# Kernel tuning notes

Measured on AMD Instinct MI355X. Metric: run time of the kernel, lower is better.

Reference implementation:

```python
import jax, jax.numpy as jnp
import numpy as np

N_NODES = 100000
N_EDGES = 800000
IN_F, H_F, OUT_F = 512, 256, 64
N_EXPERTS = 4  # k = 1


def _normalize_edges(edge_index, n):
    """gcn_norm: add self loops, symmetric D^-1/2 A D^-1/2 edge weights."""
    loop = jnp.arange(n, dtype=edge_index.dtype)
    row = jnp.concatenate([edge_index[0], loop])
    col = jnp.concatenate([edge_index[1], loop])
    w = jnp.ones(row.shape[0], dtype=jnp.float32)
    deg = jax.ops.segment_sum(w, col, num_segments=n)  # in-degree incl. self loop
    dinv = jnp.where(deg > 0, deg ** -0.5, 0.0)
    norm = dinv[row] * w * dinv[col]
    return row, col, norm


def _propagate(x, row, col, norm, n):
    # message x_j * edge_weight, scatter-add at destination col
    msgs = x[row] * norm[:, None]
    return jax.ops.segment_sum(msgs, col, num_segments=n)


def _moe_linear(x, w_gate, expert_w, expert_b):
    # eval-mode noisy top-k gating with k=1: clean logits, top-1, softmax over
    # a single logit -> gate value 1.0 for the selected expert.
    logits = x @ w_gate                         # [N, E]
    idx = jnp.argmax(logits, axis=-1)           # [N]
    gates = jax.nn.one_hot(idx, N_EXPERTS, dtype=x.dtype)  # [N, E]
    y_all = jnp.einsum('ni,eio->neo', x, expert_w) + expert_b[None]  # [N, E, H]
    return jnp.einsum('ne,neo->no', gates, y_all)


def setup_inputs() -> dict:
    key = jax.random.key(0)
    ks = jax.random.split(key, 8)
    x = jax.random.normal(ks[0], (N_NODES, IN_F), dtype=jnp.float32)
    edge_index = jax.random.randint(ks[1], (2, N_EDGES), 0, N_NODES, dtype=jnp.int64)
    w_gate = jax.random.normal(ks[2], (IN_F, N_EXPERTS), dtype=jnp.float32) * 0.05
    expert_w = jax.random.normal(ks[3], (N_EXPERTS, IN_F, H_F), dtype=jnp.float32) * (1.0 / np.sqrt(IN_F))
    expert_b = jnp.zeros((N_EXPERTS, H_F), dtype=jnp.float32)
    bias1 = jnp.zeros((H_F,), dtype=jnp.float32)
    w2 = jax.random.normal(ks[4], (H_F, OUT_F), dtype=jnp.float32) * (1.0 / np.sqrt(H_F))
    bias2 = jnp.zeros((OUT_F,), dtype=jnp.float32)
    return {"x": x, "edge_index": edge_index, "w_gate": w_gate,
            "expert_w": expert_w, "expert_b": expert_b, "bias1": bias1,
            "w2": w2, "bias2": bias2}


def reference(x, edge_index, w_gate, expert_w, expert_b, bias1, w2, bias2):
    n = x.shape[0]
    row, col, norm = _normalize_edges(edge_index, n)
    # conv1: MoE linear -> propagate -> bias
    h = _moe_linear(x, w_gate, expert_w, expert_b)
    h = _propagate(h, row, col, norm, n) + bias1
    h = jax.nn.relu(h)
    # dropout is identity at eval
    # conv2: plain GCNConv
    h = h @ w2
    h = _propagate(h, row, col, norm, n) + bias2
    return jax.nn.log_softmax(h, axis=1)
```

## Files before the change

kernel.cpp:

```cpp
#include <hip/hip_runtime.h>
#include <math.h>

typedef __bf16 bf16x8 __attribute__((ext_vector_type(8)));
typedef float f32x16 __attribute__((ext_vector_type(16)));

__device__ __forceinline__ float wave_reduce_sum(float v) {
  #pragma unroll
  for (int off = 32; off > 0; off >>= 1) v += __shfl_xor(v, off, 64);
  return v;
}
__device__ __forceinline__ float wave_reduce_max(float v) {
  #pragma unroll
  for (int off = 32; off > 0; off >>= 1) v = fmaxf(v, __shfl_xor(v, off, 64));
  return v;
}
__device__ __forceinline__ unsigned short f2bf(float f) {
  union { float f; unsigned int u; } v; v.f = f;
  unsigned int r = (v.u + 0x7FFFu + ((v.u >> 16) & 1u)) >> 16;
  return (unsigned short)r;
}
__device__ __forceinline__ float bf2f(unsigned short u) {
  union { unsigned int u; float f; } v; v.u = ((unsigned int)u) << 16;
  return v.f;
}

__global__ void k_init(int* cnt, int* meta, int N) {
  int i = blockIdx.x * blockDim.x + threadIdx.x;
  if (i < N) cnt[i] = 0;
  if (i < 32) meta[i] = 0;
}

__global__ void k_count(const int* __restrict__ col, int* __restrict__ cnt, int E) {
  int e = blockIdx.x * blockDim.x + threadIdx.x;
  if (e < E) atomicAdd(&cnt[col[e]], 1);
}

__global__ __launch_bounds__(256) void k_scanA(const int* __restrict__ cnt,
                                               int* __restrict__ incl,
                                               int* __restrict__ bsums, int N) {
  __shared__ int s[1024];
  int base = blockIdx.x * 1024;
  #pragma unroll
  for (int t = 0; t < 4; ++t) {
    int i = threadIdx.x + t * 256;
    int idx = base + i;
    s[i] = (idx < N) ? cnt[idx] : 0;
  }
  __syncthreads();
  for (int d = 1; d < 1024; d <<= 1) {
    int v[4];
    #pragma unroll
    for (int t = 0; t < 4; ++t) {
      int i = threadIdx.x + t * 256;
      v[t] = (i >= d) ? s[i - d] : 0;
    }
    __syncthreads();
    #pragma unroll
    for (int t = 0; t < 4; ++t) {
      int i = threadIdx.x + t * 256;
      s[i] += v[t];
    }
    __syncthreads();
  }
  #pragma unroll
  for (int t = 0; t < 4; ++t) {
    int i = threadIdx.x + t * 256;
    int idx = base + i;
    if (idx < N) incl[idx] = s[i];
  }
  if (threadIdx.x == 0) bsums[blockIdx.x] = s[1023];
}

__global__ __launch_bounds__(256) void k_scanB(const int* __restrict__ bsums,
                                               int* __restrict__ boff, int nb) {
  __shared__ int s[1024];
  #pragma unroll
  for (int t = 0; t < 4; ++t) {
    int i = threadIdx.x + t * 256;
    s[i] = (i < nb) ? bsums[i] : 0;
  }
  __syncthreads();
  for (int d = 1; d < 1024; d <<= 1) {
    int v[4];
    #pragma unroll
    for (int t = 0; t < 4; ++t) {
      int i = threadIdx.x + t * 256;
      v[t] = (i >= d) ? s[i - d] : 0;
    }
    __syncthreads();
    #pragma unroll
    for (int t = 0; t < 4; ++t) {
      int i = threadIdx.x + t * 256;
      s[i] += v[t];
    }
    __syncthreads();
  }
  #pragma unroll
  for (int t = 0; t < 4; ++t) {
    int i = threadIdx.x + t * 256;
    if (i < nb) boff[i] = (i == 0) ? 0 : s[i - 1];
  }
}

__global__ void k_scanC(const int* __restrict__ cnt, const int* __restrict__ incl,
                        const int* __restrict__ boff, int* __restrict__ rowptr,
                        int* __restrict__ cursor, float* __restrict__ dinv, int N, int E) {
  int i = blockIdx.x * blockDim.x + threadIdx.x;
  if (i < N) {
    int ex = incl[i] - cnt[i] + boff[i >> 10];
    rowptr[i] = ex;
    cursor[i] = ex;
    dinv[i] = rsqrtf((float)(cnt[i] + 1));
    if (i == 0) rowptr[N] = E;
  }
}

__global__ void k_scatter(const int* __restrict__ row, const int* __restrict__ col,
                          int* __restrict__ cursor, int* __restrict__ csr, int E) {
  int e = blockIdx.x * blockDim.x + threadIdx.x;
  if (e < E) {
    int c = col[e];
    int p = atomicAdd(&cursor[c], 1);
    csr[p] = row[e];
  }
}

__global__ __launch_bounds__(256) void k_gate(const float* __restrict__ x,
                                              const float* __restrict__ wg,
                                              int* __restrict__ eidx,
                                              int* __restrict__ meta,
                                              unsigned short* __restrict__ xb, int N) {
  __shared__ int lhist[4];
  int tid = threadIdx.x;
  if (tid < 4) lhist[tid] = 0;
  __syncthreads();
  int node = blockIdx.x * 16 + (tid >> 4);
  int sl = tid & 15;
  if (node < N) {
    const float* xr = x + (size_t)node * 512;
    unsigned short* xbr = xb + (size_t)node * 512;
    float l0 = 0.f, l1 = 0.f, l2 = 0.f, l3 = 0.f;
    #pragma unroll
    for (int j = 0; j < 8; ++j) {
      int q = sl + 16 * j;
      float4 xv = *(const float4*)(xr + 4 * q);
      ushort4 ov;
      ov.x = f2bf(xv.x); ov.y = f2bf(xv.y); ov.z = f2bf(xv.z); ov.w = f2bf(xv.w);
      *(ushort4*)(xbr + 4 * q) = ov;
      float4 w0 = *(const float4*)(wg + 4 * (4 * q + 0));
      float4 w1 = *(const float4*)(wg + 4 * (4 * q + 1));
      float4 w2 = *(const float4*)(wg + 4 * (4 * q + 2));
      float4 w3 = *(const float4*)(wg + 4 * (4 * q + 3));
      l0 += xv.x * w0.x + xv.y * w1.x + xv.z * w2.x + xv.w * w3.x;
      l1 += xv.x * w0.y + xv.y * w1.y + xv.z * w2.y + xv.w * w3.y;
      l2 += xv.x * w0.z + xv.y * w1.z + xv.z * w2.z + xv.w * w3.z;
      l3 += xv.x * w0.w + xv.y * w1.w + xv.z * w2.w + xv.w * w3.w;
    }
    #pragma unroll
    for (int off = 8; off > 0; off >>= 1) {
      l0 += __shfl_xor(l0, off, 64);
      l1 += __shfl_xor(l1, off, 64);
      l2 += __shfl_xor(l2, off, 64);
      l3 += __shfl_xor(l3, off, 64);
    }
    if (sl == 0) {
      int a = 0; float best = l0;
      if (l1 > best) { best = l1; a = 1; }
      if (l2 > best) { best = l2; a = 2; }
      if (l3 > best) { best = l3; a = 3; }
      eidx[node] = a;
      atomicAdd(&lhist[a], 1);
    }
  }
  __syncthreads();
  if (tid < 4 && lhist[tid] > 0) atomicAdd(&meta[tid], lhist[tid]);
}

__global__ void k_offs(int* meta) {
  if (threadIdx.x == 0 && blockIdx.x == 0) {
    int* hist = meta;
    int* eoff = meta + 4;
    int* toff = meta + 9;
    int* ecur = meta + 14;
    int s = 0, t = 0;
    eoff[0] = 0; toff[0] = 0;
    for (int e = 0; e < 4; ++e) {
      s += hist[e];
      eoff[e + 1] = s;
      t += (hist[e] + 127) / 128;
      toff[e + 1] = t;
      ecur[e] = eoff[e];
    }
  }
}

__global__ __launch_bounds__(256) void k_binscatter(const int* __restrict__ eidx,
                                                    int* __restrict__ meta,
                                                    int* __restrict__ perm, int N) {
  __shared__ int lhist[4];
  __shared__ int lbase[4];
  int tid = threadIdx.x;
  if (tid < 4) lhist[tid] = 0;
  __syncthreads();
  int n = blockIdx.x * 256 + tid;
  int e = 0, lrank = 0;
  bool valid = (n < N);
  if (valid) {
    e = eidx[n];
    lrank = atomicAdd(&lhist[e], 1);
  }
  __syncthreads();
  if (tid < 4) {
    int c = lhist[tid];
    lbase[tid] = (c > 0) ? atomicAdd(&meta[14 + tid], c) : 0;
  }
  __syncthreads();
  if (valid) perm[lbase[e] + lrank] = n;
}

__global__ __launch_bounds__(256) void k_pack(const float* __restrict__ ew,
                                              unsigned short* __restrict__ ewb) {
  int b = blockIdx.x;
  int n = threadIdx.x;
  int e = b >> 6, kc = b & 63;
  const float* src = ew + ((size_t)e * 512 + (size_t)kc * 8) * 256 + n;
  unsigned short tmp[8];
  #pragma unroll
  for (int ke = 0; ke < 8; ++ke) tmp[ke] = f2bf(src[(size_t)ke * 256]);
  *(uint4*)(ewb + ((size_t)b * 256 + n) * 8) = *(const uint4*)tmp;
}

__global__ __launch_bounds__(64) void k_pack2(const float* __restrict__ w2,
                                              unsigned short* __restrict__ w2b) {
  int kc = blockIdx.x;
  int n = threadIdx.x;
  const float* src = w2 + (size_t)kc * 8 * 64 + n;
  unsigned short tmp[8];
  #pragma unroll
  for (int ke = 0; ke < 8; ++ke) tmp[ke] = f2bf(src[(size_t)ke * 64]);
  *(uint4*)(w2b + ((size_t)kc * 64 + n) * 8) = *(const uint4*)tmp;
}

__global__ __launch_bounds__(512, 2) void k_gemm1(const unsigned short* __restrict__ xb,
                                                  const unsigned short* __restrict__ ewb,
                                                  const float* __restrict__ eb,
                                                  const int* __restrict__ perm,
                                                  const int* __restrict__ meta,
                                                  unsigned short* __restrict__ h1) {
  __shared__ __align__(16) unsigned short A_lds[8192];
  __shared__ __align__(16) unsigned short B_lds[16384];
  __shared__ int sperm[128];
  const int* eoff = meta + 4;
  const int* toff = meta + 9;
  int v = blockIdx.x;
  if (v >= toff[4]) return;
  int e = 0;
  while (v >= toff[e + 1]) ++e;
  int m0 = eoff[e] + (v - toff[e]) * 128;
  int mEnd = eoff[e + 1];
  int tid = threadIdx.x;

  if (tid < 128) {
    int m = m0 + tid;
    sperm[tid] = perm[(m < mEnd) ? m : (mEnd - 1)];
  }
  __syncthreads();

  int wave = tid >> 6, lane = tid & 63;
  int wr = wave >> 2, wc = wave & 3;
  int hi = lane >> 5, lo = lane & 31;

  f32x16 acc[2][2];
  #pragma unroll
  for (int mi = 0; mi < 2; ++mi)
    #pragma unroll
    for (int ni = 0; ni < 2; ++ni)
      #pragma unroll
      for (int r = 0; r < 16; ++r) acc[mi][ni][r] = 0.f;

  const unsigned short* arow = xb + (size_t)sperm[tid & 127] * 512;
  int kclA = tid >> 7;
  const uint4* ebase = (const uint4*)(ewb + (size_t)e * 64 * 2048);

  for (int k0 = 0; k0 < 512; k0 += 64) {
    uint4 a0 = *(const uint4*)(arow + k0 + kclA * 8);
    uint4 a1 = *(const uint4*)(arow + k0 + (kclA + 4) * 8);
    const uint4* bsrc = ebase + (size_t)(k0 >> 3) * 256;
    uint4 b0 = bsrc[tid];
    uint4 b1 = bsrc[512 + tid];
    uint4 b2 = bsrc[1024 + tid];
    uint4 b3 = bsrc[1536 + tid];
    __syncthreads();
    *(uint4*)&A_lds[((size_t)kclA * 128 + (tid & 127)) * 8] = a0;
    *(uint4*)&A_lds[((size_t)(kclA + 4) * 128 + (tid & 127)) * 8] = a1;
    *(uint4*)&B_lds[((size_t)0 * 512 + tid) * 8] = b0;
    *(uint4*)&B_lds[((size_t)1 * 512 + tid) * 8] = b1;
    *(uint4*)&B_lds[((size_t)2 * 512 + tid) * 8] = b2;
    *(uint4*)&B_lds[((size_t)3 * 512 + tid) * 8] = b3;
    __syncthreads();
    #pragma unroll
    for (int s = 0; s < 4; ++s) {
      int kcl = s * 2 + hi;
      bf16x8 a0f = *(const bf16x8*)&A_lds[((size_t)kcl * 128 + wr * 64 + lo) * 8];
      bf16x8 a1f = *(const bf16x8*)&A_lds[((size_t)kcl * 128 + wr * 64 + 32 + lo) * 8];
      bf16x8 b0f = *(const bf16x8*)&B_lds[((size_t)kcl * 256 + wc * 64 + lo) * 8];
      bf16x8 b1f = *(const bf16x8*)&B_lds[((size_t)kcl * 256 + wc * 64 + 32 + lo) * 8];
      acc[0][0] = __builtin_amdgcn_mfma_f32_32x32x16_bf16(a0f, b0f, acc[0][0], 0, 0, 0);
      acc[0][1] = __builtin_amdgcn_mfma_f32_32x32x16_bf16(a0f, b1f, acc[0][1], 0, 0, 0);
      acc[1][0] = __builtin_amdgcn_mfma_f32_32x32x16_bf16(a1f, b0f, acc[1][0], 0, 0, 0);
      acc[1][1] = __builtin_amdgcn_mfma_f32_32x32x16_bf16(a1f, b1f, acc[1][1], 0, 0, 0);
    }
  }

  #pragma unroll
  for (int ni = 0; ni < 2; ++ni) {
    int col = wc * 64 + ni * 32 + lo;
    float bias = eb[e * 256 + col];
    #pragma unroll
    for (int mi = 0; mi < 2; ++mi) {
      #pragma unroll
      for (int q = 0; q < 4; ++q) {
        #pragma unroll
        for (int j = 0; j < 4; ++j) {
          int r = j + 8 * q + 4 * hi;
          int lrow = wr * 64 + mi * 32 + r;
          if (m0 + lrow < mEnd) {
            h1[(size_t)sperm[lrow] * 256 + col] = f2bf(acc[mi][ni][q * 4 + j] + bias);
          }
        }
      }
    }
  }
}

__global__ __launch_bounds__(256) void k_prop1(const unsigned short* __restrict__ h1,
                                               const int* __restrict__ rowptr,
                                               const int* __restrict__ csr,
                                               const float* __restrict__ dinv,
                                               const float* __restrict__ bias1,
                                               unsigned short* __restrict__ hrelu, int N) {
  int c = blockIdx.x * 4 + (threadIdx.x >> 6);
  int lane = threadIdx.x & 63;
  if (c >= N) return;
  float dc = dinv[c];
  const ushort4* hr = (const ushort4*)h1;
  ushort4 sv = hr[(size_t)c * 64 + lane];
  float sl = dc * dc;
  float ax = bf2f(sv.x) * sl, ay = bf2f(sv.y) * sl, az = bf2f(sv.z) * sl, aw = bf2f(sv.w) * sl;
  int jb = rowptr[c], je = rowptr[c + 1];
  int j = jb;
  for (; j + 3 < je; j += 4) {
    int r0 = csr[j], r1 = csr[j + 1], r2 = csr[j + 2], r3 = csr[j + 3];
    float s0 = dinv[r0] * dc, s1 = dinv[r1] * dc, s2 = dinv[r2] * dc, s3 = dinv[r3] * dc;
    ushort4 h0 = hr[(size_t)r0 * 64 + lane];
    ushort4 h1v = hr[(size_t)r1 * 64 + lane];
    ushort4 h2 = hr[(size_t)r2 * 64 + lane];
    ushort4 h3v = hr[(size_t)r3 * 64 + lane];
    ax += bf2f(h0.x) * s0; ay += bf2f(h0.y) * s0; az += bf2f(h0.z) * s0; aw += bf2f(h0.w) * s0;
    ax += bf2f(h1v.x) * s1; ay += bf2f(h1v.y) * s1; az += bf2f(h1v.z) * s1; aw += bf2f(h1v.w) * s1;
    ax += bf2f(h2.x) * s2; ay += bf2f(h2.y) * s2; az += bf2f(h2.z) * s2; aw += bf2f(h2.w) * s2;
    ax += bf2f(h3v.x) * s3; ay += bf2f(h3v.y) * s3; az += bf2f(h3v.z) * s3; aw += bf2f(h3v.w) * s3;
  }
  for (; j < je; ++j) {
    int r = csr[j];
    float s = dinv[r] * dc;
    ushort4 hv = hr[(size_t)r * 64 + lane];
    ax += bf2f(hv.x) * s; ay += bf2f(hv.y) * s; az += bf2f(hv.z) * s; aw += bf2f(hv.w) * s;
  }
  float4 b = ((const float4*)bias1)[lane];
  ushort4 ov;
  ov.x = f2bf(fmaxf(ax + b.x, 0.f));
  ov.y = f2bf(fmaxf(ay + b.y, 0.f));
  ov.z = f2bf(fmaxf(az + b.z, 0.f));
  ov.w = f2bf(fmaxf(aw + b.w, 0.f));
  ((ushort4*)hrelu)[(size_t)c * 64 + lane] = ov;
}

__global__ __launch_bounds__(256, 2) void k_gemm2(const unsigned short* __restrict__ A,
                                                  const unsigned short* __restrict__ w2b,
                                                  unsigned short* __restrict__ h3, int N) {
  __shared__ __align__(16) unsigned short B_lds[16384];
  __shared__ __align__(16) unsigned short A_lds[8192];
  int tid = threadIdx.x;
  int m0 = blockIdx.x * 128;
  #pragma unroll
  for (int it = 0; it < 8; ++it)
    *(uint4*)&B_lds[((size_t)it * 256 + tid) * 8] = ((const uint4*)w2b)[it * 256 + tid];

  int wave = tid >> 6, lane = tid & 63;
  int wr = wave >> 1, wc = wave & 1;
  int hi = lane >> 5, lo = lane & 31;

  f32x16 acc[2];
  #pragma unroll
  for (int mi = 0; mi < 2; ++mi)
    #pragma unroll
    for (int r = 0; r < 16; ++r) acc[mi][r] = 0.f;

  int i = tid & 127;
  int row = m0 + i;
  if (row >= N) row = N - 1;
  const unsigned short* arow = A + (size_t)row * 256;
  int kcl0 = tid >> 7;

  for (int k0 = 0; k0 < 256; k0 += 64) {
    uint4 a[4];
    #pragma unroll
    for (int t = 0; t < 4; ++t)
      a[t] = *(const uint4*)(arow + k0 + (kcl0 + 2 * t) * 8);
    __syncthreads();
    #pragma unroll
    for (int t = 0; t < 4; ++t)
      *(uint4*)&A_lds[((size_t)(kcl0 + 2 * t) * 128 + i) * 8] = a[t];
    __syncthreads();
    #pragma unroll
    for (int s = 0; s < 4; ++s) {
      int kcl = s * 2 + hi;
      bf16x8 a0f = *(const bf16x8*)&A_lds[((size_t)kcl * 128 + wr * 64 + lo) * 8];
      bf16x8 a1f = *(const bf16x8*)&A_lds[((size_t)kcl * 128 + wr * 64 + 32 + lo) * 8];
      bf16x8 bf = *(const bf16x8*)&B_lds[(((size_t)(k0 >> 3) + kcl) * 64 + wc * 32 + lo) * 8];
      acc[0] = __builtin_amdgcn_mfma_f32_32x32x16_bf16(a0f, bf, acc[0], 0, 0, 0);
      acc[1] = __builtin_amdgcn_mfma_f32_32x32x16_bf16(a1f, bf, acc[1], 0, 0, 0);
    }
  }

  int n = wc * 32 + lo;
  #pragma unroll
  for (int mi = 0; mi < 2; ++mi) {
    #pragma unroll
    for (int q = 0; q < 4; ++q) {
      #pragma unroll
      for (int j = 0; j < 4; ++j) {
        int r = j + 8 * q + 4 * hi;
        int orow = m0 + wr * 64 + mi * 32 + r;
        if (orow < N) h3[(size_t)orow * 64 + n] = f2bf(acc[mi][q * 4 + j]);
      }
    }
  }
}

__global__ __launch_bounds__(256) void k_prop2(const unsigned short* __restrict__ h3,
                                               const int* __restrict__ rowptr,
                                               const int* __restrict__ csr,
                                               const float* __restrict__ dinv,
                                               const float* __restrict__ bias2,
                                               float* __restrict__ out, int N) {
  int c = blockIdx.x * 4 + (threadIdx.x >> 6);
  int f = threadIdx.x & 63;
  if (c >= N) return;
  float dc = dinv[c];
  float acc = bf2f(h3[(size_t)c * 64 + f]) * dc * dc;
  int jb = rowptr[c], je = rowptr[c + 1];
  int j = jb;
  for (; j + 3 < je; j += 4) {
    int r0 = csr[j], r1 = csr[j + 1], r2 = csr[j + 2], r3 = csr[j + 3];
    float s0 = dinv[r0] * dc, s1 = dinv[r1] * dc, s2 = dinv[r2] * dc, s3 = dinv[r3] * dc;
    float v0 = bf2f(h3[(size_t)r0 * 64 + f]);
    float v1 = bf2f(h3[(size_t)r1 * 64 + f]);
    float v2 = bf2f(h3[(size_t)r2 * 64 + f]);
    float v3 = bf2f(h3[(size_t)r3 * 64 + f]);
    acc += v0 * s0 + v1 * s1 + v2 * s2 + v3 * s3;
  }
  for (; j < je; ++j) {
    int r = csr[j];
    acc += bf2f(h3[(size_t)r * 64 + f]) * (dinv[r] * dc);
  }
  acc += bias2[f];
  float m = wave_reduce_max(acc);
  float ex = expf(acc - m);
  float s = wave_reduce_sum(ex);
  out[(size_t)c * 64 + f] = acc - m - logf(s);
}

extern "C" void kernel_launch(void* const* d_in, const int* in_sizes, int n_in,
                              void* d_out, int out_size, void* d_ws, size_t ws_size,
                              hipStream_t stream) {
  const float* x  = (const float*)d_in[0];
  const int*   ei = (const int*)d_in[1];
  const float* wg = (const float*)d_in[2];
  const float* ew = (const float*)d_in[3];
  const float* eb = (const float*)d_in[4];
  const float* b1 = (const float*)d_in[5];
  const float* w2 = (const float*)d_in[6];
  const float* b2 = (const float*)d_in[7];
  float* out = (float*)d_out;

  int N = in_sizes[0] / 512;
  int E = in_sizes[1] / 2;
  const int* row = ei;
  const int* col = ei + E;

  char* p = (char*)d_ws;
  auto alloc = [&](size_t bytes) -> void* {
    void* r = (void*)p;
    p += (bytes + 255) & ~(size_t)255;
    return r;
  };
  int*   cnt    = (int*)alloc((size_t)N * 4);
  int*   rowptr = (int*)alloc((size_t)(N + 1) * 4);
  int*   cursor = (int*)alloc((size_t)N * 4);
  int*   bsums  = (int*)alloc(1024 * 4);
  int*   boff   = (int*)alloc(1024 * 4);
  float* dinv   = (float*)alloc((size_t)N * 4);
  int*   eidx   = (int*)alloc((size_t)N * 4);
  int*   meta   = (int*)alloc(32 * 4);
  int*   perm   = (int*)alloc((size_t)N * 4);
  int*   csr    = (int*)alloc((size_t)E * 4);
  unsigned short* h1    = (unsigned short*)alloc((size_t)N * 256 * 2);
  unsigned short* hrelu = (unsigned short*)alloc((size_t)N * 256 * 2);
  unsigned short* h3    = (unsigned short*)alloc((size_t)N * 64 * 2);
  unsigned short* xb  = (unsigned short*)alloc((size_t)N * 512 * 2);
  unsigned short* ewb = (unsigned short*)alloc((size_t)4 * 512 * 256 * 2);
  unsigned short* w2b = (unsigned short*)alloc((size_t)256 * 64 * 2);

  int nb = (N + 1023) / 1024;

  k_init<<<(N + 255) / 256, 256, 0, stream>>>(cnt, meta, N);
  k_count<<<(E + 255) / 256, 256, 0, stream>>>(col, cnt, E);
  k_scanA<<<nb, 256, 0, stream>>>(cnt, rowptr, bsums, N);
  k_scanB<<<1, 256, 0, stream>>>(bsums, boff, nb);
  k_scanC<<<(N + 255) / 256, 256, 0, stream>>>(cnt, rowptr, boff, rowptr, cursor, dinv, N, E);
  k_scatter<<<(E + 255) / 256, 256, 0, stream>>>(row, col, cursor, csr, E);
  k_pack<<<256, 256, 0, stream>>>(ew, ewb);
  k_pack2<<<32, 64, 0, stream>>>(w2, w2b);
  k_gate<<<(N + 15) / 16, 256, 0, stream>>>(x, wg, eidx, meta, xb, N);
  k_offs<<<1, 64, 0, stream>>>(meta);
  k_binscatter<<<(N + 255) / 256, 256, 0, stream>>>(eidx, meta, perm, N);
  int ntiles = (N + 127) / 128 + 4;
  k_gemm1<<<ntiles, 512, 0, stream>>>(xb, ewb, eb, perm, meta, h1);
  k_prop1<<<(N + 3) / 4, 256, 0, stream>>>(h1, rowptr, csr, dinv, b1, hrelu, N);
  k_gemm2<<<(N + 127) / 128, 256, 0, stream>>>(hrelu, w2b, h3, N);
  k_prop2<<<(N + 3) / 4, 256, 0, stream>>>(h3, rowptr, csr, dinv, b2, out, N);
}
```

Before: 425.5 us.

## Widen gather loads in propagation kernels to 16-byte per lane, fewer lanes per node

Both sparse propagation kernels now have each lane load a 16-byte vector of eight bf16 values instead of 8 or 2 bytes. A node is handled by 32 lanes in prop1 and by 8 lanes in prop2, so each wave covers more destination nodes. The log-softmax in prop2 reduces within 8-lane groups using local max/sum plus three shuffles and writes float4 outputs. This aims to cut per-lane instruction and index-load overhead and make better use of the memory system on random gathers. The cost is higher register pressure and more divergence, since nodes sharing a wave have different degrees.

```diff
diff --git a/kernel.cpp b/kernel.cpp
--- a/kernel.cpp
+++ b/kernel.cpp
@@ -7,11 +7,6 @@
 __device__ __forceinline__ float wave_reduce_sum(float v) {
   #pragma unroll
   for (int off = 32; off > 0; off >>= 1) v += __shfl_xor(v, off, 64);
-  return v;
-}
-__device__ __forceinline__ float wave_reduce_max(float v) {
-  #pragma unroll
-  for (int off = 32; off > 0; off >>= 1) v = fmaxf(v, __shfl_xor(v, off, 64));
   return v;
 }
 __device__ __forceinline__ unsigned short f2bf(float f) {
@@ -22,6 +17,11 @@
 __device__ __forceinline__ float bf2f(unsigned short u) {
   union { unsigned int u; float f; } v; v.u = ((unsigned int)u) << 16;
   return v.f;
+}
+__device__ __forceinline__ void bf2x(unsigned int u, float& lo, float& hi) {
+  union { unsigned int u; float f; } a, b;
+  a.u = u << 16; b.u = u & 0xFFFF0000u;
+  lo = a.f; hi = b.f;
 }
 
 __global__ void k_init(int* cnt, int* meta, int N) {
@@ -339,41 +339,57 @@
                                                const float* __restrict__ dinv,
                                                const float* __restrict__ bias1,
                                                unsigned short* __restrict__ hrelu, int N) {
-  int c = blockIdx.x * 4 + (threadIdx.x >> 6);
-  int lane = threadIdx.x & 63;
+  int tid = threadIdx.x;
+  int c = blockIdx.x * 8 + (tid >> 5);
+  int l = tid & 31;
   if (c >= N) return;
   float dc = dinv[c];
-  const ushort4* hr = (const ushort4*)h1;
-  ushort4 sv = hr[(size_t)c * 64 + lane];
-  float sl = dc * dc;
-  float ax = bf2f(sv.x) * sl, ay = bf2f(sv.y) * sl, az = bf2f(sv.z) * sl, aw = bf2f(sv.w) * sl;
+  const uint4* hr = (const uint4*)h1;
+  uint4 sv = hr[(size_t)c * 32 + l];
+  float slf = dc * dc;
+  float a0, a1, a2, a3, a4, a5, a6, a7;
+  {
+    float lo, hi;
+    bf2x(sv.x, lo, hi); a0 = lo * slf; a1 = hi * slf;
+    bf2x(sv.y, lo, hi); a2 = lo * slf; a3 = hi * slf;
+    bf2x(sv.z, lo, hi); a4 = lo * slf; a5 = hi * slf;
+    bf2x(sv.w, lo, hi); a6 = lo * slf; a7 = hi * slf;
+  }
   int jb = rowptr[c], je = rowptr[c + 1];
   int j = jb;
+  #define ACC8(v, s) { float lo, hi; \
+    bf2x((v).x, lo, hi); a0 += lo * (s); a1 += hi * (s); \
+    bf2x((v).y, lo, hi); a2 += lo * (s); a3 += hi * (s); \
+    bf2x((v).z, lo, hi); a4 += lo * (s); a5 += hi * (s); \
+    bf2x((v).w, lo, hi); a6 += lo * (s); a7 += hi * (s); }
   for (; j + 3 < je; j += 4) {
     int r0 = csr[j], r1 = csr[j + 1], r2 = csr[j + 2], r3 = csr[j + 3];
     float s0 = dinv[r0] * dc, s1 = dinv[r1] * dc, s2 = dinv[r2] * dc, s3 = dinv[r3] * dc;
-    ushort4 h0 = hr[(size_t)r0 * 64 + lane];
-    ushort4 h1v = hr[(size_t)r1 * 64 + lane];
-    ushort4 h2 = hr[(size_t)r2 * 64 + lane];
-    ushort4 h3v = hr[(size_t)r3 * 64 + lane];
-    ax += bf2f(h0.x) * s0; ay += bf2f(h0.y) * s0; az += bf2f(h0.z) * s0; aw += bf2f(h0.w) * s0;
-    ax += bf2f(h1v.x) * s1; ay += bf2f(h1v.y) * s1; az += bf2f(h1v.z) * s1; aw += bf2f(h1v.w) * s1;
-    ax += bf2f(h2.x) * s2; ay += bf2f(h2.y) * s2; az += bf2f(h2.z) * s2; aw += bf2f(h2.w) * s2;
-    ax += bf2f(h3v.x) * s3; ay += bf2f(h3v.y) * s3; az += bf2f(h3v.z) * s3; aw += bf2f(h3v.w) * s3;
+    uint4 v0 = hr[(size_t)r0 * 32 + l];
+    uint4 v1 = hr[(size_t)r1 * 32 + l];
+    uint4 v2 = hr[(size_t)r2 * 32 + l];
+    uint4 v3 = hr[(size_t)r3 * 32 + l];
+    ACC8(v0, s0); ACC8(v1, s1); ACC8(v2, s2); ACC8(v3, s3);
   }
   for (; j < je; ++j) {
     int r = csr[j];
     float s = dinv[r] * dc;
-    ushort4 hv = hr[(size_t)r * 64 + lane];
-    ax += bf2f(hv.x) * s; ay += bf2f(hv.y) * s; az += bf2f(hv.z) * s; aw += bf2f(hv.w) * s;
-  }
-  float4 b = ((const float4*)bias1)[lane];
-  ushort4 ov;
-  ov.x = f2bf(fmaxf(ax + b.x, 0.f));
-  ov.y = f2bf(fmaxf(ay + b.y, 0.f));
-  ov.z = f2bf(fmaxf(az + b.z, 0.f));
-  ov.w = f2bf(fmaxf(aw + b.w, 0.f));
-  ((ushort4*)hrelu)[(size_t)c * 64 + lane] = ov;
+    uint4 v = hr[(size_t)r * 32 + l];
+    ACC8(v, s);
+  }
+  #undef ACC8
+  float4 b01 = *(const float4*)(bias1 + l * 8);
+  float4 b23 = *(const float4*)(bias1 + l * 8 + 4);
+  a0 = fmaxf(a0 + b01.x, 0.f); a1 = fmaxf(a1 + b01.y, 0.f);
+  a2 = fmaxf(a2 + b01.z, 0.f); a3 = fmaxf(a3 + b01.w, 0.f);
+  a4 = fmaxf(a4 + b23.x, 0.f); a5 = fmaxf(a5 + b23.y, 0.f);
+  a6 = fmaxf(a6 + b23.z, 0.f); a7 = fmaxf(a7 + b23.w, 0.f);
+  uint4 ov;
+  ov.x = ((unsigned int)f2bf(a1) << 16) | f2bf(a0);
+  ov.y = ((unsigned int)f2bf(a3) << 16) | f2bf(a2);
+  ov.z = ((unsigned int)f2bf(a5) << 16) | f2bf(a4);
+  ov.w = ((unsigned int)f2bf(a7) << 16) | f2bf(a6);
+  ((uint4*)hrelu)[(size_t)c * 32 + l] = ov;
 }
 
 __global__ __launch_bounds__(256, 2) void k_gemm2(const unsigned short* __restrict__ A,
@@ -445,31 +461,62 @@
                                                const float* __restrict__ dinv,
                                                const float* __restrict__ bias2,
                                                float* __restrict__ out, int N) {
-  int c = blockIdx.x * 4 + (threadIdx.x >> 6);
-  int f = threadIdx.x & 63;
+  int tid = threadIdx.x;
+  int c = blockIdx.x * 32 + (tid >> 3);
+  int l = tid & 7;
   if (c >= N) return;
   float dc = dinv[c];
-  float acc = bf2f(h3[(size_t)c * 64 + f]) * dc * dc;
+  const uint4* hr = (const uint4*)h3;
+  uint4 sv = hr[(size_t)c * 8 + l];
+  float slf = dc * dc;
+  float a0, a1, a2, a3, a4, a5, a6, a7;
+  {
+    float lo, hi;
+    bf2x(sv.x, lo, hi); a0 = lo * slf; a1 = hi * slf;
+    bf2x(sv.y, lo, hi); a2 = lo * slf; a3 = hi * slf;
+    bf2x(sv.z, lo, hi); a4 = lo * slf; a5 = hi * slf;
+    bf2x(sv.w, lo, hi); a6 = lo * slf; a7 = hi * slf;
+  }
   int jb = rowptr[c], je = rowptr[c + 1];
   int j = jb;
+  #define ACC8(v, s) { float lo, hi; \
+    bf2x((v).x, lo, hi); a0 += lo * (s); a1 += hi * (s); \
+    bf2x((v).y, lo, hi); a2 += lo * (s); a3 += hi * (s); \
+    bf2x((v).z, lo, hi); a4 += lo * (s); a5 += hi * (s); \
+    bf2x((v).w, lo, hi); a6 += lo * (s); a7 += hi * (s); }
   for (; j + 3 < je; j += 4) {
     int r0 = csr[j], r1 = csr[j + 1], r2 = csr[j + 2], r3 = csr[j + 3];
     float s0 = dinv[r0] * dc, s1 = dinv[r1] * dc, s2 = dinv[r2] * dc, s3 = dinv[r3] * dc;
-    float v0 = bf2f(h3[(size_t)r0 * 64 + f]);
-    float v1 = bf2f(h3[(size_t)r1 * 64 + f]);
-    float v2 = bf2f(h3[(size_t)r2 * 64 + f]);
-    float v3 = bf2f(h3[(size_t)r3 * 64 + f]);
-    acc += v0 * s0 + v1 * s1 + v2 * s2 + v3 * s3;
+    uint4 v0 = hr[(size_t)r0 * 8 + l];
+    uint4 v1 = hr[(size_t)r1 * 8 + l];
+    uint4 v2 = hr[(size_t)r2 * 8 + l];
+    uint4 v3 = hr[(size_t)r3 * 8 + l];
+    ACC8(v0, s0); ACC8(v1, s1); ACC8(v2, s2); ACC8(v3, s3);
   }
   for (; j < je; ++j) {
     int r = csr[j];
-    acc += bf2f(h3[(size_t)r * 64 + f]) * (dinv[r] * dc);
-  }
-  acc += bias2[f];
-  float m = wave_reduce_max(acc);
-  float ex = expf(acc - m);
-  float s = wave_reduce_sum(ex);
-  out[(size_t)c * 64 + f] = acc - m - logf(s);
+    float s = dinv[r] * dc;
+    uint4 v = hr[(size_t)r * 8 + l];
+    ACC8(v, s);
+  }
+  #undef ACC8
+  float4 b01 = *(const float4*)(bias2 + l * 8);
+  float4 b23 = *(const float4*)(bias2 + l * 8 + 4);
+  a0 += b01.x; a1 += b01.y; a2 += b01.z; a3 += b01.w;
+  a4 += b23.x; a5 += b23.y; a6 += b23.z; a7 += b23.w;
+  float m = fmaxf(fmaxf(fmaxf(a0, a1), fmaxf(a2, a3)), fmaxf(fmaxf(a4, a5), fmaxf(a6, a7)));
+  #pragma unroll
+  for (int off = 4; off > 0; off >>= 1) m = fmaxf(m, __shfl_xor(m, off, 64));
+  float s = expf(a0 - m) + expf(a1 - m) + expf(a2 - m) + expf(a3 - m)
+          + expf(a4 - m) + expf(a5 - m) + expf(a6 - m) + expf(a7 - m);
+  #pragma unroll
+  for (int off = 4; off > 0; off >>= 1) s += __shfl_xor(s, off, 64);
+  float ls = m + logf(s);
+  float* orow = out + (size_t)c * 64 + l * 8;
+  float4 o0 = make_float4(a0 - ls, a1 - ls, a2 - ls, a3 - ls);
+  float4 o1 = make_float4(a4 - ls, a5 - ls, a6 - ls, a7 - ls);
+  *(float4*)orow = o0;
+  *(float4*)(orow + 4) = o1;
 }
 
 extern "C" void kernel_launch(void* const* d_in, const int* in_sizes, int n_in,
@@ -528,7 +575,7 @@
   k_binscatter<<<(N + 255) / 256, 256, 0, stream>>>(eidx, meta, perm, N);
   int ntiles = (N + 127) / 128 + 4;
   k_gemm1<<<ntiles, 512, 0, stream>>>(xb, ewb, eb, perm, meta, h1);
-  k_prop1<<<(N + 3) / 4, 256, 0, stream>>>(h1, rowptr, csr, dinv, b1, hrelu, N);
+  k_prop1<<<(N + 7) / 8, 256, 0, stream>>>(h1, rowptr, csr, dinv, b1, hrelu, N);
   k_gemm2<<<(N + 127) / 128, 256, 0, stream>>>(hrelu, w2b, h3, N);
-  k_prop2<<<(N + 3) / 4, 256, 0, stream>>>(h3, rowptr, csr, dinv, b2, out, N);
-}
+  k_prop2<<<(N + 31) / 32, 256, 0, stream>>>(h3, rowptr, csr, dinv, b2, out, N);
+}
```

Result: faster. 395.1 us (-7.2%).
